# Optimization experiments

Hardware: AMD Instinct MI355X
Metric: run time of the kernel (lower is better)

## Reference

```python
import jax, jax.numpy as jnp
import numpy as np

NUM_RELATIONS = 8
DROP_P = 0.2


def rgcn_layer(x, W, root, b, edge_index, edge_type, num_relations):
    # x: [N,F], W: [R,F,O], root: [F,O], b: [O]
    # edge_index: [2,E] (row 0 = source, row 1 = target), edge_type: [E]
    src, dst = edge_index[0], edge_index[1]
    N = x.shape[0]
    O = W.shape[2]
    # Transform all nodes under every relation once: [R,N,O]
    transformed = jnp.einsum('nf,rfo->rno', x, W)
    msg = transformed[edge_type, src]  # [E,O] gather per edge
    # mean aggregation per relation: per-(relation,target) in-degree
    deg = jnp.zeros((num_relations, N), x.dtype).at[edge_type, dst].add(1.0)
    coef = (1.0 / jnp.clip(deg, 1.0))[edge_type, dst]  # [E]
    agg = jnp.zeros((N, O), x.dtype).at[dst].add(msg * coef[:, None])
    return agg + x @ root + b


def setup_inputs() -> dict:
    key = jax.random.key(0)
    ks = jax.random.split(key, 10)
    N, E, F, H, O, R = 50000, 400000, 128, 128, 64, NUM_RELATIONS
    x = jax.random.normal(ks[0], (N, F), jnp.float32)
    edge_index = jax.random.randint(ks[1], (2, E), 0, N, jnp.int64)
    edge_type = jax.random.randint(ks[2], (E,), 0, R, jnp.int64)
    s = 1.0 / np.sqrt(F)
    W1 = jax.random.normal(ks[3], (R, F, H), jnp.float32) * s
    root1 = jax.random.normal(ks[4], (F, H), jnp.float32) * s
    b1 = jnp.zeros((H,), jnp.float32)
    sh = 1.0 / np.sqrt(H)
    W2 = jax.random.normal(ks[5], (R, H, O), jnp.float32) * sh
    root2 = jax.random.normal(ks[6], (H, O), jnp.float32) * sh
    b2 = jnp.zeros((O,), jnp.float32)
    # inverted dropout mask (training mode, p=0.2), precomputed for determinism
    keep = jax.random.bernoulli(ks[7], 1.0 - DROP_P, (N, H))
    drop_mask = keep.astype(jnp.float32) / (1.0 - DROP_P)
    return {"x": x, "edge_index": edge_index, "edge_type": edge_type,
            "W1": W1, "root1": root1, "b1": b1,
            "W2": W2, "root2": root2, "b2": b2, "drop_mask": drop_mask}


def reference(x, edge_index, edge_type, W1, root1, b1, W2, root2, b2, drop_mask):
    h = rgcn_layer(x, W1, root1, b1, edge_index, edge_type, NUM_RELATIONS)
    h = jax.nn.relu(h) * drop_mask  # fused relu + dropout
    out = rgcn_layer(h, W2, root2, b2, edge_index, edge_type, NUM_RELATIONS)
    return out
```

## Files before the change

kernel.cpp:

```cpp
#include <hip/hip_runtime.h>
#include <hip/hip_bf16.h>
#include <stdint.h>

typedef __attribute__((ext_vector_type(8))) short bf16x8;
typedef __attribute__((ext_vector_type(4))) float f32x4;

__device__ __forceinline__ unsigned f2bf(float f){
  unsigned u = __builtin_bit_cast(unsigned, f);
  return (u + 0x7FFFu + ((u >> 16) & 1u)) >> 16;
}
__device__ __forceinline__ float bf2f(unsigned s){
  unsigned u = s << 16; return __builtin_bit_cast(float, u);
}
__device__ __forceinline__ void add8(float* a, uint4 g){
  a[0] += bf2f(g.x & 0xFFFFu); a[1] += bf2f(g.x >> 16);
  a[2] += bf2f(g.y & 0xFFFFu); a[3] += bf2f(g.y >> 16);
  a[4] += bf2f(g.z & 0xFFFFu); a[5] += bf2f(g.z >> 16);
  a[6] += bf2f(g.w & 0xFFFFu); a[7] += bf2f(g.w >> 16);
}
__device__ __forceinline__ void stage16(const void* g, void* l){
  __builtin_amdgcn_global_load_lds((const __attribute__((address_space(1))) void*)g,
                                   (__attribute__((address_space(3))) void*)l, 16, 0, 0);
}

__global__ void k_combo(const float* __restrict__ x,
                        const float* __restrict__ W1, const float* __restrict__ r1,
                        const float* __restrict__ W2, const float* __restrict__ r2,
                        const int* __restrict__ ei, const int* __restrict__ et,
                        short* __restrict__ Wt1, short* __restrict__ Wt2,
                        uint2* __restrict__ xb, int* __restrict__ degr,
                        int N, int E, int WB, int XB){
  int b = blockIdx.x, tid = threadIdx.x;
  if (b < WB){
    int t = b * 256 + tid;
    if (t < 128 * 1152){
      int o = t / 1152, ka = t - o * 1152, ph = ka >> 7, k = ka & 127;
      float v = (ph < 8) ? W1[(ph * 128 + k) * 128 + o] : r1[k * 128 + o];
      int dst = ph * 16384 + o * 128 + (((k >> 3) ^ (o & 7)) << 3) + (k & 7);
      Wt1[dst] = (short)f2bf(v);
    } else if (t < 128 * 1152 + 64 * 1152){
      int t2 = t - 128 * 1152;
      int o = t2 / 1152, ka = t2 - o * 1152, ph = ka >> 7, k = ka & 127;
      float v = (ph < 8) ? W2[(ph * 128 + k) * 64 + o] : r2[k * 64 + o];
      int dst = ph * 8192 + o * 128 + (((k >> 3) ^ (o & 7)) << 3) + (k & 7);
      Wt2[dst] = (short)f2bf(v);
    }
  } else if (b < WB + XB){
    int t = (b - WB) * 256 + tid;
    if (t < N * 32){
      float4 v = reinterpret_cast<const float4*>(x)[t];
      uint2 o;
      o.x = f2bf(v.x) | (f2bf(v.y) << 16);
      o.y = f2bf(v.z) | (f2bf(v.w) << 16);
      xb[t] = o;
    }
  } else {
    int e = (b - WB - XB) * 256 + tid;
    if (e < E){
      unsigned dst = (unsigned)ei[E + e];
      int rel = et[e] & 7;
      if (dst < (unsigned)N) atomicAdd(&degr[rel * N + dst], 1);
    }
  }
}

__global__ void k_scan1(const int* __restrict__ cnt, int* __restrict__ incl,
                        int* __restrict__ bsum, int M){
  __shared__ int s[256];
  int i = blockIdx.x * 256 + threadIdx.x;
  int v = (i < M) ? cnt[i] : 0;
  s[threadIdx.x] = v; __syncthreads();
  for (int d = 1; d < 256; d <<= 1){
    int t = (threadIdx.x >= d) ? s[threadIdx.x - d] : 0;
    __syncthreads();
    s[threadIdx.x] += t;
    __syncthreads();
  }
  if (i < M) incl[i] = s[threadIdx.x];
  if (threadIdx.x == 255) bsum[blockIdx.x] = s[255];
}
__global__ void k_scan2(int* bsum, int NB){
  __shared__ int s[256];
  int t = threadIdx.x;
  int carry = 0;
  for (int c0 = 0; c0 < NB; c0 += 256){
    int i = c0 + t;
    int v = (i < NB) ? bsum[i] : 0;
    s[t] = v; __syncthreads();
    for (int d = 1; d < 256; d <<= 1){
      int u = (t >= d) ? s[t - d] : 0;
      __syncthreads();
      s[t] += u;
      __syncthreads();
    }
    if (i < NB) bsum[i] = s[t] + carry;
    int tot = s[255];
    __syncthreads();
    carry += tot;
  }
}
__global__ void k_fin(const int* __restrict__ cnt, const int* __restrict__ incl,
                      const int* __restrict__ bsum, int* __restrict__ offs,
                      unsigned* __restrict__ pmeta, int M){
  int i = blockIdx.x * 256 + threadIdx.x;
  if (i >= M) return;
  int base = (blockIdx.x > 0) ? bsum[blockIdx.x - 1] : 0;
  int off = base + incl[i] - cnt[i];
  offs[i] = off;
  int c = cnt[i]; if (c > 4095) c = 4095;
  pmeta[i] = (unsigned)off | ((unsigned)c << 20);
}

__global__ void k_fill(const int* __restrict__ ei, const int* __restrict__ et,
                       const int* __restrict__ offs, int* __restrict__ fill,
                       unsigned short* __restrict__ idx, int E, int N){
  int e = blockIdx.x * 256 + threadIdx.x;
  if (e >= E) return;
  unsigned src = (unsigned)ei[e];
  unsigned dst = (unsigned)ei[E + e];
  int rel = et[e] & 7;
  if (dst < (unsigned)N){
    int key = rel * N + (int)dst;
    int p = atomicAdd(&fill[key], 1);
    idx[offs[key] + p] = (unsigned short)src;
  }
}

template<int NF, int MODE>
__global__ __launch_bounds__(256, 2)
void k_fused(const short* __restrict__ feat, const unsigned* __restrict__ pmeta,
             const unsigned short* __restrict__ idx2, const short* __restrict__ Wt,
             const float* __restrict__ bias, const float* __restrict__ mask,
             void* __restrict__ outp, int N){
  constexpr int BN = NF * 16;
  constexpr int NPW = NF / 4;
  __shared__ char sA[9 * 16 * 256];
  __shared__ char sB[BN * 256];
  int tid = threadIdx.x, lane = tid & 63, wave = tid >> 6;
  int row0 = blockIdx.x * 16;

  {
    int q4 = BN * 64;
    const char* gsrc = (const char*)Wt;
    #pragma unroll
    for (int i = 0; i < BN / 16; i++){
      int base = wave * q4 + i * 1024;
      stage16(gsrc + base + lane * 16, sB + base);
    }
  }

  {
    int r = tid >> 4, l = tid & 15;
    int dstj = row0 + r;
    bool vd = dstj < N;
    int dsafe = vd ? dstj : 0;
    unsigned m[8];
    #pragma unroll
    for (int ph = 0; ph < 8; ph++) m[ph] = vd ? pmeta[ph * N + dstj] : 0u;
    int s0[8], s1[8];
    #pragma unroll
    for (int ph = 0; ph < 8; ph++){
      int cnt = (int)(m[ph] >> 20), base = (int)(m[ph] & 0xFFFFFu);
      s0[ph] = (cnt > 0) ? (int)idx2[base] : 0;
      s1[ph] = (cnt > 1) ? (int)idx2[base + 1] : 0;
    }
    uint4 g0[8], g1[8], gr;
    #pragma unroll
    for (int ph = 0; ph < 8; ph++)
      g0[ph] = *reinterpret_cast<const uint4*>(feat + (size_t)s0[ph] * 128 + l * 8);
    #pragma unroll
    for (int ph = 0; ph < 8; ph++)
      g1[ph] = *reinterpret_cast<const uint4*>(feat + (size_t)s1[ph] * 128 + l * 8);
    gr = *reinterpret_cast<const uint4*>(feat + (size_t)dsafe * 128 + l * 8);

    int swz = (l ^ (r & 7)) << 4;
    #pragma unroll
    for (int ph = 0; ph < 8; ph++){
      int cnt = (int)(m[ph] >> 20), base = (int)(m[ph] & 0xFFFFFu);
      uint4 ov = {0u, 0u, 0u, 0u};
      if (cnt > 0){
        float a[8];
        a[0]=bf2f(g0[ph].x&0xFFFFu); a[1]=bf2f(g0[ph].x>>16);
        a[2]=bf2f(g0[ph].y&0xFFFFu); a[3]=bf2f(g0[ph].y>>16);
        a[4]=bf2f(g0[ph].z&0xFFFFu); a[5]=bf2f(g0[ph].z>>16);
        a[6]=bf2f(g0[ph].w&0xFFFFu); a[7]=bf2f(g0[ph].w>>16);
        if (cnt > 1) add8(a, g1[ph]);
        for (int i = 2; i < cnt; i++){
          int s = (int)idx2[base + i];
          uint4 gi = *reinterpret_cast<const uint4*>(feat + (size_t)s * 128 + l * 8);
          add8(a, gi);
        }
        float inv = 1.0f / (float)cnt;
        ov.x = f2bf(a[0]*inv) | (f2bf(a[1]*inv) << 16);
        ov.y = f2bf(a[2]*inv) | (f2bf(a[3]*inv) << 16);
        ov.z = f2bf(a[4]*inv) | (f2bf(a[5]*inv) << 16);
        ov.w = f2bf(a[6]*inv) | (f2bf(a[7]*inv) << 16);
      }
      *reinterpret_cast<uint4*>(sA + ph * 4096 + r * 256 + swz) = ov;
    }
    *reinterpret_cast<uint4*>(sA + 8 * 4096 + r * 256 + swz) = gr;
  }

  f32x4 acc[NPW];
  f32x4 z = {0.f, 0.f, 0.f, 0.f};
  #pragma unroll
  for (int nn = 0; nn < NPW; nn++) acc[nn] = z;
  int r16 = lane & 15, q = lane >> 4;

  for (int ph = 0; ph < 9; ph++){
    asm volatile("s_waitcnt vmcnt(0)" ::: "memory");
    __syncthreads();
    #pragma unroll
    for (int kk = 0; kk < 4; kk++){
      int ch = ((kk * 4 + q) ^ (r16 & 7)) << 4;
      bf16x8 av = *reinterpret_cast<const bf16x8*>(sA + ph * 4096 + r16 * 256 + ch);
      #pragma unroll
      for (int nn = 0; nn < NPW; nn++){
        int o = (wave * NPW + nn) * 16 + r16;
        bf16x8 bv = *reinterpret_cast<const bf16x8*>(sB + o * 256 + ch);
        acc[nn] = __builtin_amdgcn_mfma_f32_16x16x32_bf16(av, bv, acc[nn], 0, 0, 0);
      }
    }
    __syncthreads();
    if (ph < 8){
      int q4 = BN * 64;
      const char* gsrc = (const char*)Wt + (size_t)(ph + 1) * BN * 256;
      #pragma unroll
      for (int i = 0; i < BN / 16; i++){
        int base = wave * q4 + i * 1024;
        stage16(gsrc + base + lane * 16, sB + base);
      }
    }
  }

  #pragma unroll
  for (int nn = 0; nn < NPW; nn++){
    int col = (wave * NPW + nn) * 16 + r16;
    float bv = bias[col];
    #pragma unroll
    for (int j = 0; j < 4; j++){
      int row = row0 + (q << 2) + j;
      if (row < N){
        float v = acc[nn][j] + bv;
        if (MODE == 1){
          v = fmaxf(v, 0.f) * mask[(size_t)row * 128 + col];
          reinterpret_cast<short*>(outp)[(size_t)row * 128 + col] = (short)f2bf(v);
        } else {
          reinterpret_cast<float*>(outp)[(size_t)row * BN + col] = v;
        }
      }
    }
  }
}

extern "C" void kernel_launch(void* const* d_in, const int* in_sizes, int n_in,
                              void* d_out, int out_size, void* d_ws, size_t ws_size,
                              hipStream_t stream){
  const float* x    = (const float*)d_in[0];
  const int*   ei   = (const int*)d_in[1];
  const int*   et   = (const int*)d_in[2];
  const float* W1   = (const float*)d_in[3];
  const float* r1   = (const float*)d_in[4];
  const float* b1   = (const float*)d_in[5];
  const float* W2   = (const float*)d_in[6];
  const float* r2   = (const float*)d_in[7];
  const float* b2   = (const float*)d_in[8];
  const float* mask = (const float*)d_in[9];
  int N = in_sizes[0] / 128;
  int E = in_sizes[2];
  int M8 = 8 * N;

  char* ws = (char*)d_ws;
  short*    xb    = (short*)(ws + 0);
  short*    hb    = (short*)(ws + 12800000);
  short*    Wt1   = (short*)(ws + 25600000);
  short*    Wt2   = (short*)(ws + 25894912);
  int*      degr  = (int*)(ws + 26042368);
  int*      fill  = (int*)(ws + 27642368);
  int*      offs2 = (int*)(ws + 29242368);
  int*      incl  = (int*)(ws + 30842368);
  unsigned* pmeta = (unsigned*)(ws + 32442368);
  int*      bsum  = (int*)(ws + 34042368);
  unsigned short* idx2 = (unsigned short*)(ws + 34050560);
  if (ws_size < (size_t)34050560 + (size_t)E * 2 + 64) return;

  hipMemsetAsync(degr, 0, (size_t)M8 * 8, stream);

  int WB = (128*1152 + 64*1152 + 255) / 256;
  int XB = (N * 32 + 255) / 256;
  int EB = (E + 255) / 256;
  int NB = (M8 + 255) / 256;
  k_combo<<<WB + XB + EB, 256, 0, stream>>>(x, W1, r1, W2, r2, ei, et,
                                            Wt1, Wt2, (uint2*)xb, degr, N, E, WB, XB);
  k_scan1<<<NB, 256, 0, stream>>>(degr, incl, bsum, M8);
  k_scan2<<<1, 256, 0, stream>>>(bsum, NB);
  k_fin<<<NB, 256, 0, stream>>>(degr, incl, bsum, offs2, pmeta, M8);
  k_fill<<<EB, 256, 0, stream>>>(ei, et, offs2, fill, idx2, E, N);

  int G = (N + 15) / 16;
  k_fused<8, 1><<<G, 256, 0, stream>>>(xb, pmeta, idx2, Wt1, b1, mask, hb, N);
  k_fused<4, 2><<<G, 256, 0, stream>>>(hb, pmeta, idx2, Wt2, b2, nullptr, d_out, N);
}
```

Before: 331.4 us.

## Load weights into registers directly, single-pass scan, bf16 mask, raise occupancy

Several changes land together. The weight tile is no longer staged through LDS: weights are laid out in MFMA fragment order and each wave loads its B operands from global memory into double-buffered registers, which drops the per-phase barriers and the sB buffer. The three-kernel prefix scan becomes one kernel that takes block bases from an atomic counter; offsets stay correct, but the bucket order is no longer deterministic. The dropout mask is converted to bf16 ahead of time to halve its reads in the fused kernel, which adds mask rounding and an extra conversion pass, and launch bounds move to 3 blocks per CU.

```diff
diff --git a/kernel.cpp b/kernel.cpp
--- a/kernel.cpp
+++ b/kernel.cpp
@@ -18,32 +18,28 @@
   a[4] += bf2f(g.z & 0xFFFFu); a[5] += bf2f(g.z >> 16);
   a[6] += bf2f(g.w & 0xFFFFu); a[7] += bf2f(g.w >> 16);
 }
-__device__ __forceinline__ void stage16(const void* g, void* l){
-  __builtin_amdgcn_global_load_lds((const __attribute__((address_space(1))) void*)g,
-                                   (__attribute__((address_space(3))) void*)l, 16, 0, 0);
-}
-
-__global__ void k_combo(const float* __restrict__ x,
+
+__global__ void k_combo(const float* __restrict__ x, const float* __restrict__ mask,
                         const float* __restrict__ W1, const float* __restrict__ r1,
                         const float* __restrict__ W2, const float* __restrict__ r2,
                         const int* __restrict__ ei, const int* __restrict__ et,
                         short* __restrict__ Wt1, short* __restrict__ Wt2,
-                        uint2* __restrict__ xb, int* __restrict__ degr,
-                        int N, int E, int WB, int XB){
+                        uint2* __restrict__ xb, uint2* __restrict__ maskb,
+                        int* __restrict__ degr, int N, int E, int WB, int XB){
   int b = blockIdx.x, tid = threadIdx.x;
   if (b < WB){
     int t = b * 256 + tid;
     if (t < 128 * 1152){
       int o = t / 1152, ka = t - o * 1152, ph = ka >> 7, k = ka & 127;
+      int kk = k >> 5, q = (k >> 3) & 3, j = k & 7;
       float v = (ph < 8) ? W1[(ph * 128 + k) * 128 + o] : r1[k * 128 + o];
-      int dst = ph * 16384 + o * 128 + (((k >> 3) ^ (o & 7)) << 3) + (k & 7);
-      Wt1[dst] = (short)f2bf(v);
+      Wt1[(((ph * 4 + kk) * 4 + q) * 128 + o) * 8 + j] = (short)f2bf(v);
     } else if (t < 128 * 1152 + 64 * 1152){
       int t2 = t - 128 * 1152;
       int o = t2 / 1152, ka = t2 - o * 1152, ph = ka >> 7, k = ka & 127;
+      int kk = k >> 5, q = (k >> 3) & 3, j = k & 7;
       float v = (ph < 8) ? W2[(ph * 128 + k) * 64 + o] : r2[k * 64 + o];
-      int dst = ph * 8192 + o * 128 + (((k >> 3) ^ (o & 7)) << 3) + (k & 7);
-      Wt2[dst] = (short)f2bf(v);
+      Wt2[(((ph * 4 + kk) * 4 + q) * 64 + o) * 8 + j] = (short)f2bf(v);
     }
   } else if (b < WB + XB){
     int t = (b - WB) * 256 + tid;
@@ -53,6 +49,13 @@
       o.x = f2bf(v.x) | (f2bf(v.y) << 16);
       o.y = f2bf(v.z) | (f2bf(v.w) << 16);
       xb[t] = o;
+    } else if (t < N * 64){
+      int t2 = t - N * 32;
+      float4 v = reinterpret_cast<const float4*>(mask)[t2];
+      uint2 o;
+      o.x = f2bf(v.x) | (f2bf(v.y) << 16);
+      o.y = f2bf(v.z) | (f2bf(v.w) << 16);
+      maskb[t2] = o;
     }
   } else {
     int e = (b - WB - XB) * 256 + tid;
@@ -64,9 +67,10 @@
   }
 }
 
-__global__ void k_scan1(const int* __restrict__ cnt, int* __restrict__ incl,
-                        int* __restrict__ bsum, int M){
+__global__ void k_scan(const int* __restrict__ cnt, int* __restrict__ gcnt,
+                       int* __restrict__ offs, unsigned* __restrict__ pmeta, int M){
   __shared__ int s[256];
+  __shared__ int sbase;
   int i = blockIdx.x * 256 + threadIdx.x;
   int v = (i < M) ? cnt[i] : 0;
   s[threadIdx.x] = v; __syncthreads();
@@ -76,39 +80,14 @@
     s[threadIdx.x] += t;
     __syncthreads();
   }
-  if (i < M) incl[i] = s[threadIdx.x];
-  if (threadIdx.x == 255) bsum[blockIdx.x] = s[255];
-}
-__global__ void k_scan2(int* bsum, int NB){
-  __shared__ int s[256];
-  int t = threadIdx.x;
-  int carry = 0;
-  for (int c0 = 0; c0 < NB; c0 += 256){
-    int i = c0 + t;
-    int v = (i < NB) ? bsum[i] : 0;
-    s[t] = v; __syncthreads();
-    for (int d = 1; d < 256; d <<= 1){
-      int u = (t >= d) ? s[t - d] : 0;
-      __syncthreads();
-      s[t] += u;
-      __syncthreads();
-    }
-    if (i < NB) bsum[i] = s[t] + carry;
-    int tot = s[255];
-    __syncthreads();
-    carry += tot;
-  }
-}
-__global__ void k_fin(const int* __restrict__ cnt, const int* __restrict__ incl,
-                      const int* __restrict__ bsum, int* __restrict__ offs,
-                      unsigned* __restrict__ pmeta, int M){
-  int i = blockIdx.x * 256 + threadIdx.x;
-  if (i >= M) return;
-  int base = (blockIdx.x > 0) ? bsum[blockIdx.x - 1] : 0;
-  int off = base + incl[i] - cnt[i];
-  offs[i] = off;
-  int c = cnt[i]; if (c > 4095) c = 4095;
-  pmeta[i] = (unsigned)off | ((unsigned)c << 20);
+  if (threadIdx.x == 255) sbase = atomicAdd(gcnt, s[255]);
+  __syncthreads();
+  if (i < M){
+    int off = sbase + s[threadIdx.x] - v;
+    offs[i] = off;
+    int c = v; if (c > 4095) c = 4095;
+    pmeta[i] = (unsigned)off | ((unsigned)c << 20);
+  }
 }
 
 __global__ void k_fill(const int* __restrict__ ei, const int* __restrict__ et,
@@ -127,27 +106,16 @@
 }
 
 template<int NF, int MODE>
-__global__ __launch_bounds__(256, 2)
+__global__ __launch_bounds__(256, 3)
 void k_fused(const short* __restrict__ feat, const unsigned* __restrict__ pmeta,
              const unsigned short* __restrict__ idx2, const short* __restrict__ Wt,
-             const float* __restrict__ bias, const float* __restrict__ mask,
+             const float* __restrict__ bias, const short* __restrict__ maskb,
              void* __restrict__ outp, int N){
   constexpr int BN = NF * 16;
   constexpr int NPW = NF / 4;
   __shared__ char sA[9 * 16 * 256];
-  __shared__ char sB[BN * 256];
   int tid = threadIdx.x, lane = tid & 63, wave = tid >> 6;
   int row0 = blockIdx.x * 16;
-
-  {
-    int q4 = BN * 64;
-    const char* gsrc = (const char*)Wt;
-    #pragma unroll
-    for (int i = 0; i < BN / 16; i++){
-      int base = wave * q4 + i * 1024;
-      stage16(gsrc + base + lane * 16, sB + base);
-    }
-  }
 
   {
     int r = tid >> 4, l = tid & 15;
@@ -201,41 +169,47 @@
     *reinterpret_cast<uint4*>(sA + 8 * 4096 + r * 256 + swz) = gr;
   }
 
+  int r16 = lane & 15, q = lane >> 4;
+  int obase = wave * NPW * 16 + r16;
+  bf16x8 bb[2][4][NPW];
+  #pragma unroll
+  for (int kk = 0; kk < 4; kk++)
+    #pragma unroll
+    for (int nn = 0; nn < NPW; nn++)
+      bb[0][kk][nn] = *reinterpret_cast<const bf16x8*>(
+          Wt + ((size_t)(kk * 4 + q) * BN + obase + nn * 16) * 8);
+
+  __syncthreads();
+
   f32x4 acc[NPW];
   f32x4 z = {0.f, 0.f, 0.f, 0.f};
   #pragma unroll
   for (int nn = 0; nn < NPW; nn++) acc[nn] = z;
-  int r16 = lane & 15, q = lane >> 4;
-
+
+  #pragma unroll
   for (int ph = 0; ph < 9; ph++){
-    asm volatile("s_waitcnt vmcnt(0)" ::: "memory");
-    __syncthreads();
+    if (ph < 8){
+      #pragma unroll
+      for (int kk = 0; kk < 4; kk++)
+        #pragma unroll
+        for (int nn = 0; nn < NPW; nn++)
+          bb[(ph + 1) & 1][kk][nn] = *reinterpret_cast<const bf16x8*>(
+              Wt + ((size_t)(((ph + 1) * 4 + kk) * 4 + q) * BN + obase + nn * 16) * 8);
+    }
     #pragma unroll
     for (int kk = 0; kk < 4; kk++){
       int ch = ((kk * 4 + q) ^ (r16 & 7)) << 4;
       bf16x8 av = *reinterpret_cast<const bf16x8*>(sA + ph * 4096 + r16 * 256 + ch);
       #pragma unroll
-      for (int nn = 0; nn < NPW; nn++){
-        int o = (wave * NPW + nn) * 16 + r16;
-        bf16x8 bv = *reinterpret_cast<const bf16x8*>(sB + o * 256 + ch);
-        acc[nn] = __builtin_amdgcn_mfma_f32_16x16x32_bf16(av, bv, acc[nn], 0, 0, 0);
-      }
-    }
-    __syncthreads();
-    if (ph < 8){
-      int q4 = BN * 64;
-      const char* gsrc = (const char*)Wt + (size_t)(ph + 1) * BN * 256;
-      #pragma unroll
-      for (int i = 0; i < BN / 16; i++){
-        int base = wave * q4 + i * 1024;
-        stage16(gsrc + base + lane * 16, sB + base);
-      }
+      for (int nn = 0; nn < NPW; nn++)
+        acc[nn] = __builtin_amdgcn_mfma_f32_16x16x32_bf16(av, bb[ph & 1][kk][nn],
+                                                          acc[nn], 0, 0, 0);
     }
   }
 
   #pragma unroll
   for (int nn = 0; nn < NPW; nn++){
-    int col = (wave * NPW + nn) * 16 + r16;
+    int col = obase + nn * 16;
     float bv = bias[col];
     #pragma unroll
     for (int j = 0; j < 4; j++){
@@ -243,7 +217,7 @@
       if (row < N){
         float v = acc[nn][j] + bv;
         if (MODE == 1){
-          v = fmaxf(v, 0.f) * mask[(size_t)row * 128 + col];
+          v = fmaxf(v, 0.f) * bf2f((unsigned)(unsigned short)maskb[(size_t)row * 128 + col]);
           reinterpret_cast<short*>(outp)[(size_t)row * 128 + col] = (short)f2bf(v);
         } else {
           reinterpret_cast<float*>(outp)[(size_t)row * BN + col] = v;
@@ -273,31 +247,30 @@
   char* ws = (char*)d_ws;
   short*    xb    = (short*)(ws + 0);
   short*    hb    = (short*)(ws + 12800000);
-  short*    Wt1   = (short*)(ws + 25600000);
-  short*    Wt2   = (short*)(ws + 25894912);
-  int*      degr  = (int*)(ws + 26042368);
-  int*      fill  = (int*)(ws + 27642368);
-  int*      offs2 = (int*)(ws + 29242368);
-  int*      incl  = (int*)(ws + 30842368);
-  unsigned* pmeta = (unsigned*)(ws + 32442368);
-  int*      bsum  = (int*)(ws + 34042368);
-  unsigned short* idx2 = (unsigned short*)(ws + 34050560);
-  if (ws_size < (size_t)34050560 + (size_t)E * 2 + 64) return;
-
-  hipMemsetAsync(degr, 0, (size_t)M8 * 8, stream);
+  short*    maskb = (short*)(ws + 25600000);
+  short*    Wt1   = (short*)(ws + 38400000);
+  short*    Wt2   = (short*)(ws + 38694912);
+  int*      degr  = (int*)(ws + 38842368);
+  int*      fill  = (int*)(ws + 40442368);
+  int*      gcnt  = (int*)(ws + 42042368);
+  int*      offs2 = (int*)(ws + 42042432);
+  unsigned* pmeta = (unsigned*)(ws + 43642432);
+  unsigned short* idx2 = (unsigned short*)(ws + 45242432);
+  if (ws_size < (size_t)45242432 + (size_t)E * 2 + 64) return;
+
+  hipMemsetAsync(degr, 0, (size_t)M8 * 8 + 64, stream);
 
   int WB = (128*1152 + 64*1152 + 255) / 256;
-  int XB = (N * 32 + 255) / 256;
+  int XB = (N * 64 + 255) / 256;
   int EB = (E + 255) / 256;
   int NB = (M8 + 255) / 256;
-  k_combo<<<WB + XB + EB, 256, 0, stream>>>(x, W1, r1, W2, r2, ei, et,
-                                            Wt1, Wt2, (uint2*)xb, degr, N, E, WB, XB);
-  k_scan1<<<NB, 256, 0, stream>>>(degr, incl, bsum, M8);
-  k_scan2<<<1, 256, 0, stream>>>(bsum, NB);
-  k_fin<<<NB, 256, 0, stream>>>(degr, incl, bsum, offs2, pmeta, M8);
+  k_combo<<<WB + XB + EB, 256, 0, stream>>>(x, mask, W1, r1, W2, r2, ei, et,
+                                            Wt1, Wt2, (uint2*)xb, (uint2*)maskb,
+                                            degr, N, E, WB, XB);
+  k_scan<<<NB, 256, 0, stream>>>(degr, gcnt, offs2, pmeta, M8);
   k_fill<<<EB, 256, 0, stream>>>(ei, et, offs2, fill, idx2, E, N);
 
   int G = (N + 15) / 16;
-  k_fused<8, 1><<<G, 256, 0, stream>>>(xb, pmeta, idx2, Wt1, b1, mask, hb, N);
+  k_fused<8, 1><<<G, 256, 0, stream>>>(xb, pmeta, idx2, Wt1, b1, maskb, hb, N);
   k_fused<4, 2><<<G, 256, 0, stream>>>(hb, pmeta, idx2, Wt2, b2, nullptr, d_out, N);
 }
```

Result: faster. 285.9 us (-13.7%).
